# Kernel optimization log

Hardware: AMD Instinct MI355X
Metric: run time of the kernel (lower is better)

Reference implementation:

```python
import jax, jax.numpy as jnp
import numpy as np

B, S, D = 4, 2048, 1024
H = 16
DK = D // H  # 64, dim_k == dim_v
FF = 4096
EPS = 1e-5


def layer_norm(x, g, b):
    mu = jnp.mean(x, axis=-1, keepdims=True)
    var = jnp.mean(jnp.square(x - mu), axis=-1, keepdims=True)
    return (x - mu) * jax.lax.rsqrt(var + EPS) * g + b


def setup_inputs() -> dict:
    key = jax.random.key(0)
    ks = jax.random.split(key, 16)
    s = 0.02
    return {
        "src": jax.random.normal(ks[0], (B, S, D), jnp.float32),
        # per-head Q/K/V projections (stacked over heads)
        "wq": jax.random.normal(ks[1], (H, D, DK), jnp.float32) * s,
        "bq": jnp.zeros((H, DK), jnp.float32),
        "wk": jax.random.normal(ks[2], (H, D, DK), jnp.float32) * s,
        "bk": jnp.zeros((H, DK), jnp.float32),
        "wv": jax.random.normal(ks[3], (H, D, DK), jnp.float32) * s,
        "bv": jnp.zeros((H, DK), jnp.float32),
        # output projection: concat(H*DK) -> D
        "wo": jax.random.normal(ks[4], (H * DK, D), jnp.float32) * s,
        "bo": jnp.zeros((D,), jnp.float32),
        "ln1_g": jnp.ones((D,), jnp.float32),
        "ln1_b": jnp.zeros((D,), jnp.float32),
        # FFN
        "w1": jax.random.normal(ks[5], (D, FF), jnp.float32) * s,
        "b1": jnp.zeros((FF,), jnp.float32),
        "w2": jax.random.normal(ks[6], (FF, D), jnp.float32) * s,
        "b2": jnp.zeros((D,), jnp.float32),
        "ln2_g": jnp.ones((D,), jnp.float32),
        "ln2_b": jnp.zeros((D,), jnp.float32),
    }


def reference(src, wq, bq, wk, bk, wv, bv, wo, bo, ln1_g, ln1_b,
              w1, b1, w2, b2, ln2_g, ln2_b):
    # per-head projections: [B,S,D] x [H,D,K] -> [B,H,S,K]
    q = jnp.einsum('bsd,hdk->bhsk', src, wq) + bq[None, :, None, :]
    k = jnp.einsum('bsd,hdk->bhsk', src, wk) + bk[None, :, None, :]
    v = jnp.einsum('bsd,hdk->bhsk', src, wv) + bv[None, :, None, :]
    scale = 1.0 / jnp.sqrt(jnp.float32(DK))
    scores = jnp.einsum('bhsk,bhtk->bhst', q, k) * scale  # [B,H,S,S]
    attn = jax.nn.softmax(scores, axis=-1)
    o = jnp.einsum('bhst,bhtv->bhsv', attn, v)            # [B,H,S,DK]
    o = o.transpose(0, 2, 1, 3).reshape(B, S, H * DK)      # concat heads
    attn_out = o @ wo + bo
    x = layer_norm(src + attn_out, ln1_g, ln1_b)
    ff = jax.nn.relu(x @ w1 + b1) @ w2 + b2
    return layer_norm(x + ff, ln2_g, ln2_b)
```

## Files before the change

kernel.cpp:

```cpp
#include <hip/hip_runtime.h>

typedef __bf16 bf16;
typedef __bf16 bf16x8 __attribute__((ext_vector_type(8)));
typedef __bf16 bf16x4 __attribute__((ext_vector_type(4)));
typedef float  f32x4  __attribute__((ext_vector_type(4)));
typedef float  f32x16 __attribute__((ext_vector_type(16)));
typedef unsigned int u32;
typedef int i32x2 __attribute__((ext_vector_type(2)));
typedef int i32x4 __attribute__((ext_vector_type(4)));

#define NB 4
#define NS 2048
#define ND 1024
#define NH 16
#define NDK 64
#define NFF 4096
#define NM (NB*NS)

#define QSCALE 0.18033688f

__device__ __forceinline__ void load_lds16(const void* g, void* l) {
  __builtin_amdgcn_global_load_lds(
      (const __attribute__((address_space(1))) void*)g,
      (__attribute__((address_space(3))) void*)l, 16, 0, 0);
}

__device__ __forceinline__ u32 pack2(float a, float b) {
  union { bf16 h[2]; u32 u; } z;
  z.h[0] = (bf16)a; z.h[1] = (bf16)b;
  return z.u;
}

__device__ __forceinline__ i32x2 pswap(u32 a, u32 b) {
#if __has_builtin(__builtin_amdgcn_permlane32_swap)
  return __builtin_amdgcn_permlane32_swap((int)a, (int)b, false, false);
#else
  u32 x = a, y = b;
  asm volatile("v_permlane32_swap_b32 %0, %1" : "+v"(x), "+v"(y));
  i32x2 r; r[0] = (int)x; r[1] = (int)y; return r;
#endif
}

__global__ __launch_bounds__(256)
void cvt_f32_bf16(const float* __restrict__ in, bf16* __restrict__ out, int n) {
  int i = (blockIdx.x * 256 + threadIdx.x) * 4;
  if (i < n) {
    float4 v = *(const float4*)&in[i];
    bf16x4 o;
    o[0] = (bf16)v.x; o[1] = (bf16)v.y; o[2] = (bf16)v.z; o[3] = (bf16)v.w;
    *(bf16x4*)&out[i] = o;
  }
}

__global__ __launch_bounds__(256)
void transpose_cvt(const float* __restrict__ in, bf16* __restrict__ out,
                   int R, int C, size_t in_bs, size_t out_bs) {
  __shared__ float t[32][33];
  int bx = blockIdx.x, by = blockIdx.y, bz = blockIdx.z;
  const float* ip = in + (size_t)bz * in_bs + (size_t)(bx * 32) * C + by * 32;
  bf16* op = out + (size_t)bz * out_bs + (size_t)(by * 32) * R + bx * 32;
  int x = threadIdx.x & 31, y = threadIdx.x >> 5;
#pragma unroll
  for (int yy = 0; yy < 32; yy += 8)
    t[y + yy][x] = ip[(size_t)(y + yy) * C + x];
  __syncthreads();
#pragma unroll
  for (int yy = 0; yy < 32; yy += 8)
    op[(size_t)(y + yy) * R + x] = (bf16)t[x][y + yy];
}

__global__ __launch_bounds__(256)
void transpose_v(const bf16* __restrict__ v, bf16* __restrict__ vT) {
  __shared__ bf16 t[64][72];
  int st = blockIdx.x;
  int bh = blockIdx.y;
  const bf16* ip = v + ((size_t)bh * NS + st * 64) * NDK;
  bf16* op = vT + (size_t)bh * NDK * NS + st * 64;
  int tid = threadIdx.x;
#pragma unroll
  for (int c = tid; c < 512; c += 256) {
    int r = c >> 3, q = c & 7;
    bf16x8 d = *(const bf16x8*)&ip[(size_t)r * NDK + q * 8];
#pragma unroll
    for (int j = 0; j < 8; j++) t[r][q * 8 + j] = d[j];
  }
  __syncthreads();
#pragma unroll
  for (int c = tid; c < 512; c += 256) {
    int dv = c >> 3, sq = c & 7;
    bf16x8 d;
#pragma unroll
    for (int j = 0; j < 8; j++) d[j] = t[sq * 8 + j][dv];
    *(bf16x8*)&op[(size_t)dv * NS + sq * 8] = d;
  }
}

#define BAR()  __builtin_amdgcn_s_barrier()
#define LGKM0() do { asm volatile("s_waitcnt lgkmcnt(0)" ::: "memory"); \
                     __builtin_amdgcn_sched_barrier(0); } while (0)

template<int BN, int EPI>
__global__ __launch_bounds__(512, 2)
void gemm8p(const bf16* __restrict__ A, const bf16* __restrict__ Bt,
            const float* __restrict__ bias0, const float* __restrict__ bias1,
            const float* __restrict__ bias2, void* __restrict__ out0,
            int M, int N, int K) {
  constexpr int NFR = BN / 64;
  __shared__ __align__(16) bf16 lA[2][256 * 64];
  __shared__ __align__(16) bf16 lB[2][BN * 64];

  const int tid = threadIdx.x, lane = tid & 63, w = tid >> 6;
  const int wr = w >> 2, wn = w & 3;
  const int blane = lane & 15, glane = lane >> 4;

  const int nwg = gridDim.x;
  const int cpx = nwg >> 3;
  const int bid = blockIdx.x;
  const int swzb = (bid & 7) * cpx + (bid >> 3);
  const int gridM = M >> 8;
  const int bm = (swzb % gridM) * 256;
  const int bn = (swzb / gridM) * BN;

  f32x4 acc[8][NFR] = {};
  bf16x8 aF[8], bF[2 * NFR];

  auto stageA = [&](int kt, int h, int b) {
#pragma unroll
    for (int j = 0; j < 2; j++) {
      int ch = w * 128 + j * 64 + lane;
      int r = h * 128 + (ch >> 3), s = ch & 7;
      load_lds16(A + (size_t)(bm + r) * K + kt * 64 + ((s ^ (r & 7)) * 8),
                 &lA[b][(h * 1024 + ch) * 8]);
    }
  };
  auto stageB = [&](int kt, int h, int b) {
    if constexpr (BN == 256) {
#pragma unroll
      for (int j = 0; j < 2; j++) {
        int ch = w * 128 + j * 64 + lane;
        int r = h * 128 + (ch >> 3), s = ch & 7;
        load_lds16(Bt + (size_t)(bn + r) * K + kt * 64 + ((s ^ (r & 7)) * 8),
                   &lB[b][(h * 1024 + ch) * 8]);
      }
    } else {
      int ch = w * 64 + lane;
      int r = h * 64 + (ch >> 3), s = ch & 7;
      load_lds16(Bt + (size_t)(bn + r) * K + kt * 64 + ((s ^ (r & 7)) * 8),
                 &lB[b][(h * 512 + ch) * 8]);
    }
  };
  auto vmwait = [&]() {
    if constexpr (BN == 256) asm volatile("s_waitcnt vmcnt(6)" ::: "memory");
    else                     asm volatile("s_waitcnt vmcnt(4)" ::: "memory");
  };
  auto ldA = [&](int mh, int b) {
#pragma unroll
    for (int mf = 0; mf < 4; mf++)
#pragma unroll
      for (int ks = 0; ks < 2; ks++) {
        int r = wr * 128 + mh * 64 + mf * 16 + blane;
        int s = (ks * 4 + glane) ^ (r & 7);
        aF[mf * 2 + ks] = *(const bf16x8*)&lA[b][r * 64 + s * 8];
      }
  };
  auto ldBh = [&](int nh, int b) {
#pragma unroll
    for (int nq = 0; nq < NFR / 2; nq++)
#pragma unroll
      for (int ks = 0; ks < 2; ks++) {
        int nf = nh * (NFR / 2) + nq;
        int r = wn * (NFR * 16) + nf * 16 + blane;
        int s = (ks * 4 + glane) ^ (r & 7);
        bF[nf * 2 + ks] = *(const bf16x8*)&lB[b][r * 64 + s * 8];
      }
  };

#define MMAQ(mh, nh)  do {                                                  \
    __builtin_amdgcn_s_setprio(1);                                          \
    _Pragma("unroll")                                                       \
    for (int mf = 0; mf < 4; mf++)                                          \
      _Pragma("unroll")                                                     \
      for (int nq = 0; nq < NFR / 2; nq++)                                  \
        _Pragma("unroll")                                                   \
        for (int ks = 0; ks < 2; ks++)                                      \
          acc[(mh) * 4 + mf][(nh) * (NFR / 2) + nq] =                       \
            __builtin_amdgcn_mfma_f32_16x16x32_bf16(                        \
              aF[mf * 2 + ks], bF[((nh) * (NFR / 2) + nq) * 2 + ks],        \
              acc[(mh) * 4 + mf][(nh) * (NFR / 2) + nq], 0, 0, 0);          \
    __builtin_amdgcn_s_setprio(0);                                          \
  } while (0)

  stageB(0, 0, 0); stageB(0, 1, 0); stageA(0, 0, 0); stageA(0, 1, 0);
  stageB(1, 0, 1); stageB(1, 1, 1); stageA(1, 0, 1);
  vmwait();
  BAR();

  const int NT = K >> 6;
  for (int u = 0; u < NT; u += 2) {
    const int t2 = (u + 2 < NT) ? u + 2 : u;
    const int t3 = (u + 3 < NT) ? u + 3 : u + 1;
    ldA(0, 0); ldBh(0, 0);
    stageA(u + 1, 1, 1);
    BAR(); LGKM0(); MMAQ(0, 0); BAR();
    ldBh(1, 0);
    stageB(t2, 0, 0);
    BAR(); LGKM0(); MMAQ(0, 1); BAR();
    ldA(1, 0);
    stageB(t2, 1, 0);
    BAR(); LGKM0(); MMAQ(1, 1); BAR();
    stageA(t2, 0, 0);
    BAR(); MMAQ(1, 0); vmwait(); BAR();
    ldA(0, 1); ldBh(0, 1);
    stageA(t2, 1, 0);
    BAR(); LGKM0(); MMAQ(0, 0); BAR();
    ldBh(1, 1);
    stageB(t3, 0, 1);
    BAR(); LGKM0(); MMAQ(0, 1); BAR();
    ldA(1, 1);
    stageB(t3, 1, 1);
    BAR(); LGKM0(); MMAQ(1, 1); BAR();
    stageA(t3, 0, 1);
    BAR(); MMAQ(1, 0); vmwait(); BAR();
  }

#pragma unroll
  for (int am = 0; am < 8; am++) {
#pragma unroll
    for (int nf = 0; nf < NFR; nf++) {
      int col = bn + wn * (NFR * 16) + nf * 16 + blane;
      int rowb = bm + wr * 128 + (am >> 2) * 64 + (am & 3) * 16 + glane * 4;
      if (EPI == 0) {
        int sel = col >> 10;
        int hh = (col & 1023) >> 6;
        int dv = col & 63;
        const float* bp = (sel == 0) ? bias0 : (sel == 1) ? bias1 : bias2;
        float bias = bp[col & 1023];
        float sc = (sel == 0) ? QSCALE : 1.0f;
        bf16* outb = (bf16*)out0 + (size_t)sel * NB * NH * NS * NDK;
#pragma unroll
        for (int i = 0; i < 4; i++) {
          int row = rowb + i;
          int b_ = row >> 11, s_ = row & 2047;
          outb[(((size_t)(b_ * NH + hh) * NS + s_) * NDK) + dv] = (bf16)((acc[am][nf][i] + bias) * sc);
        }
      } else if (EPI == 1) {
        float bias = bias0[col];
#pragma unroll
        for (int i = 0; i < 4; i++) {
          float v = acc[am][nf][i] + bias;
          v = v > 0.f ? v : 0.f;
          ((bf16*)out0)[(size_t)(rowb + i) * N + col] = (bf16)v;
        }
      } else {
        float bias = bias0[col];
#pragma unroll
        for (int i = 0; i < 4; i++)
          ((float*)out0)[(size_t)(rowb + i) * N + col] = acc[am][nf][i] + bias;
      }
    }
  }
#undef MMAQ
}

__global__ __launch_bounds__(512)
void flash_attn7(const bf16* __restrict__ q, const bf16* __restrict__ k,
                 const bf16* __restrict__ vT, bf16* __restrict__ o) {
  __shared__ __align__(16) bf16 lK[2][64 * 64];
  __shared__ __align__(16) bf16 lV[2][64 * 64];
  const int tid = threadIdx.x, lane = tid & 63, w = tid >> 6;
  const int ql = lane & 31, hi = lane >> 5;

  const int id = blockIdx.x;
  const int xcd = id & 7, sseq = id >> 3;
  const int bh = xcd * 8 + (sseq >> 3);
  const int qt = sseq & 7;

  const size_t hb = (size_t)bh * NS * NDK;
  const int qrow = qt * 256 + w * 32 + ql;

  bf16x8 qf[4];
#pragma unroll
  for (int ks = 0; ks < 4; ks++)
    qf[ks] = *(const bf16x8*)&q[hb + (size_t)qrow * NDK + ks * 16 + hi * 8];

  const int sr = tid >> 3, sc = ((tid & 7) ^ (sr & 7)) * 8;
  const bf16* ksrc = k  + hb + (size_t)sr * NDK + sc;
  const bf16* vsrc = vT + hb + (size_t)sr * NS  + sc;

  f32x16 o0 = {}, o1 = {};
  float ls0 = 0.f, ls1 = 0.f, ls2 = 0.f, ls3 = 0.f;
  const int swz = (ql & 7) << 4;

  {
    i32x4 rk = *(const i32x4*)ksrc;
    i32x4 rv = *(const i32x4*)vsrc;
    *(i32x4*)&lK[0][tid * 8] = rk;
    *(i32x4*)&lV[0][tid * 8] = rv;
  }
  asm volatile("s_waitcnt lgkmcnt(0)" ::: "memory");
  __builtin_amdgcn_sched_barrier(0);
  __builtin_amdgcn_s_barrier();

  const char* lKc = (const char*)&lK[0][0];
  const char* lVc = (const char*)&lV[0][0];

  for (int t = 0; t < NS / 64; t++) {
    const int cur = t & 1;
    const char* Kb = lKc + cur * 8192;
    const char* Vb = lVc + cur * 8192;

    i32x4 nk, nv;
    const bool pf = (t < NS / 64 - 1);
    if (pf) {
      nk = *(const i32x4*)(ksrc + (size_t)(t + 1) * 64 * NDK);
      nv = *(const i32x4*)(vsrc + (t + 1) * 64);
    }

    f32x16 st0 = {}, st1 = {};
    __builtin_amdgcn_s_setprio(1);
#pragma unroll
    for (int ks = 0; ks < 4; ks++) {
      int byt = (32 * ks + 16 * hi) ^ swz;
      bf16x8 kf0 = *(const bf16x8*)(Kb + ql * 128 + byt);
      bf16x8 kf1 = *(const bf16x8*)(Kb + (32 + ql) * 128 + byt);
      st0 = __builtin_amdgcn_mfma_f32_32x32x16_bf16(kf0, qf[ks], st0, 0, 0, 0);
      st1 = __builtin_amdgcn_mfma_f32_32x32x16_bf16(kf1, qf[ks], st1, 0, 0, 0);
    }
    __builtin_amdgcn_s_setprio(0);

#pragma unroll
    for (int r = 0; r < 16; r += 4) {
      float p00 = exp2f(st0[r]),     p01 = exp2f(st0[r + 1]);
      float p02 = exp2f(st0[r + 2]), p03 = exp2f(st0[r + 3]);
      float p10 = exp2f(st1[r]),     p11 = exp2f(st1[r + 1]);
      float p12 = exp2f(st1[r + 2]), p13 = exp2f(st1[r + 3]);
      st0[r] = p00; st0[r + 1] = p01; st0[r + 2] = p02; st0[r + 3] = p03;
      st1[r] = p10; st1[r + 1] = p11; st1[r + 2] = p12; st1[r + 3] = p13;
      ls0 += p00 + p10; ls1 += p01 + p11;
      ls2 += p02 + p12; ls3 += p03 + p13;
    }

#pragma unroll
    for (int tt = 0; tt < 2; tt++) {
      f32x16 stv = (tt == 0) ? st0 : st1;
      u32 wv[8];
#pragma unroll
      for (int i = 0; i < 8; i++) wv[i] = pack2(stv[2 * i], stv[2 * i + 1]);
#pragma unroll
      for (int kk = 0; kk < 2; kk++) {
        const int base = 4 * kk;
        i32x2 e0 = pswap(wv[base + 0], wv[base + 2]);
        i32x2 e1 = pswap(wv[base + 1], wv[base + 3]);
        union { u32 u[4]; bf16x8 v; } pf_;
        pf_.u[0] = (u32)e0[0];
        pf_.u[1] = (u32)e1[0];
        pf_.u[2] = (u32)e0[1];
        pf_.u[3] = (u32)e1[1];
        const int ks = 2 * tt + kk;
        int vbyt = (32 * ks + 16 * hi) ^ swz;
        bf16x8 vf0 = *(const bf16x8*)(Vb + ql * 128 + vbyt);
        bf16x8 vf1 = *(const bf16x8*)(Vb + (32 + ql) * 128 + vbyt);
        __builtin_amdgcn_s_setprio(1);
        o0 = __builtin_amdgcn_mfma_f32_32x32x16_bf16(vf0, pf_.v, o0, 0, 0, 0);
        o1 = __builtin_amdgcn_mfma_f32_32x32x16_bf16(vf1, pf_.v, o1, 0, 0, 0);
        __builtin_amdgcn_s_setprio(0);
      }
    }

    if (pf) {
      *(i32x4*)&lK[cur ^ 1][tid * 8] = nk;
      *(i32x4*)&lV[cur ^ 1][tid * 8] = nv;
    }
    asm volatile("s_waitcnt lgkmcnt(0)" ::: "memory");
    __builtin_amdgcn_sched_barrier(0);
    __builtin_amdgcn_s_barrier();
  }

  float ls = (ls0 + ls1) + (ls2 + ls3);
  float lR;
  {
    i32x2 sr2 = pswap((u32)__float_as_int(ls), (u32)__float_as_int(ls));
    float lsp = __int_as_float(hi ? sr2[0] : sr2[1]);
    float lo_ = hi ? lsp : ls, hi_ = hi ? ls : lsp;
    lR = lo_ + hi_;
  }
  float invl = 1.0f / lR;
  int b_ = bh >> 4, h_ = bh & 15;
  bf16* ob = o + ((size_t)(b_ * NS + qrow) * (NH * NDK)) + h_ * NDK;
#pragma unroll
  for (int rp = 0; rp < 8; rp++) {
    int dv = 8 * (rp >> 1) + 2 * (rp & 1) + 4 * hi;
    *(u32*)&ob[dv]      = pack2(o0[2 * rp] * invl, o0[2 * rp + 1] * invl);
    *(u32*)&ob[dv + 32] = pack2(o1[2 * rp] * invl, o1[2 * rp + 1] * invl);
  }
}

template<int WB>
__global__ __launch_bounds__(256)
void ln_res(const float* __restrict__ a, const float* __restrict__ b,
            const float* __restrict__ g, const float* __restrict__ be,
            float* __restrict__ y, bf16* __restrict__ yb) {
  int row = blockIdx.x;
  int tid = threadIdx.x;
  const float4* a4 = (const float4*)(a + (size_t)row * ND);
  const float4* b4 = (const float4*)(b + (size_t)row * ND);
  float4 av = a4[tid], bv = b4[tid];
  float x0 = av.x + bv.x, x1 = av.y + bv.y, x2 = av.z + bv.z, x3 = av.w + bv.w;
  float s = x0 + x1 + x2 + x3;
  float qq_ = x0 * x0 + x1 * x1 + x2 * x2 + x3 * x3;
#pragma unroll
  for (int d = 1; d < 64; d <<= 1) { s += __shfl_xor(s, d); qq_ += __shfl_xor(qq_, d); }
  __shared__ float ss[4], sq[4];
  int w = tid >> 6, lane = tid & 63;
  if (lane == 0) { ss[w] = s; sq[w] = qq_; }
  __syncthreads();
  s = ss[0] + ss[1] + ss[2] + ss[3];
  qq_ = sq[0] + sq[1] + sq[2] + sq[3];
  float mu = s * (1.0f / ND);
  float var = qq_ * (1.0f / ND) - mu * mu;
  float rs = 1.0f / sqrtf(var + 1e-5f);
  const float4* g4 = (const float4*)g;
  const float4* e4 = (const float4*)be;
  float4 gv = g4[tid], ev = e4[tid];
  float o0 = (x0 - mu) * rs * gv.x + ev.x;
  float o1 = (x1 - mu) * rs * gv.y + ev.y;
  float o2 = (x2 - mu) * rs * gv.z + ev.z;
  float o3 = (x3 - mu) * rs * gv.w + ev.w;
  float4 ov = {o0, o1, o2, o3};
  *(float4*)(y + (size_t)row * ND + tid * 4) = ov;
  if (WB) {
    bf16x4 wv;
    wv[0] = (bf16)o0; wv[1] = (bf16)o1; wv[2] = (bf16)o2; wv[3] = (bf16)o3;
    *(bf16x4*)&yb[(size_t)row * ND + tid * 4] = wv;
  }
}

extern "C" void kernel_launch(void* const* d_in, const int* in_sizes, int n_in,
                              void* d_out, int out_size, void* d_ws, size_t ws_size,
                              hipStream_t stream) {
  const float* src = (const float*)d_in[0];
  const float* wq  = (const float*)d_in[1];
  const float* bq  = (const float*)d_in[2];
  const float* wk  = (const float*)d_in[3];
  const float* bk  = (const float*)d_in[4];
  const float* wv  = (const float*)d_in[5];
  const float* bv  = (const float*)d_in[6];
  const float* wo  = (const float*)d_in[7];
  const float* bo  = (const float*)d_in[8];
  const float* g1  = (const float*)d_in[9];
  const float* be1 = (const float*)d_in[10];
  const float* w1  = (const float*)d_in[11];
  const float* b1  = (const float*)d_in[12];
  const float* w2  = (const float*)d_in[13];
  const float* b2  = (const float*)d_in[14];
  const float* g2  = (const float*)d_in[15];
  const float* be2 = (const float*)d_in[16];

  char* ws = (char*)d_ws;
  bf16*  srcb  = (bf16*)(ws + 0);
  bf16*  wqkvT = (bf16*)(ws + 16777216);
  bf16*  woT   = (bf16*)(ws + 23068672);
  bf16*  w1T   = (bf16*)(ws + 25165824);
  bf16*  w2T   = (bf16*)(ws + 33554432);
  bf16*  qkv   = (bf16*)(ws + 41943040);
  bf16*  vT    = (bf16*)(ws + 92274688);
  bf16*  attno = (bf16*)(ws + 109051904);
  float* tmpf  = (float*)(ws + 125829120);
  float* x     = (float*)(ws + 159383552);
  bf16*  xb    = (bf16*)(ws + 192937984);
  bf16*  hbuf  = qkv;

  const size_t QKVSZ = (size_t)NB * NH * NS * NDK;

  cvt_f32_bf16<<<8192, 256, 0, stream>>>(src, srcb, NM * ND);
  transpose_cvt<<<dim3(32, 2, 16), 256, 0, stream>>>(wq, wqkvT,               1024, 64, 65536, 65536);
  transpose_cvt<<<dim3(32, 2, 16), 256, 0, stream>>>(wk, wqkvT + 1024 * 1024, 1024, 64, 65536, 65536);
  transpose_cvt<<<dim3(32, 2, 16), 256, 0, stream>>>(wv, wqkvT + 2048 * 1024, 1024, 64, 65536, 65536);
  transpose_cvt<<<dim3(32, 32, 1), 256, 0, stream>>>(wo, woT, 1024, 1024, 0, 0);
  transpose_cvt<<<dim3(32, 128, 1), 256, 0, stream>>>(w1, w1T, 1024, 4096, 0, 0);
  transpose_cvt<<<dim3(128, 32, 1), 256, 0, stream>>>(w2, w2T, 4096, 1024, 0, 0);

  gemm8p<256, 0><<<384, 512, 0, stream>>>(srcb, wqkvT, bq, bk, bv, qkv, NM, 3072, 1024);
  transpose_v<<<dim3(32, 64), 256, 0, stream>>>(qkv + 2 * QKVSZ, vT);
  flash_attn7<<<512, 512, 0, stream>>>(qkv, qkv + QKVSZ, vT, attno);
  gemm8p<128, 2><<<256, 512, 0, stream>>>(attno, woT, bo, nullptr, nullptr, tmpf, NM, 1024, 1024);
  ln_res<1><<<8192, 256, 0, stream>>>(src, tmpf, g1, be1, x, xb);
  gemm8p<256, 1><<<512, 512, 0, stream>>>(xb, w1T, b1, nullptr, nullptr, hbuf, NM, 4096, 1024);
  gemm8p<128, 2><<<256, 512, 0, stream>>>(hbuf, w2T, b2, nullptr, nullptr, tmpf, NM, 1024, 4096);
  ln_res<0><<<8192, 256, 0, stream>>>(x, tmpf, g2, be2, (float*)d_out, nullptr);
}
```

Measured before the change: 457.5 us.

## Store projection GEMM outputs in bf16 and shrink attention blocks to 256 threads

```diff
diff --git a/kernel.cpp b/kernel.cpp
--- a/kernel.cpp
+++ b/kernel.cpp
@@ -251,19 +251,24 @@
           v = v > 0.f ? v : 0.f;
           ((bf16*)out0)[(size_t)(rowb + i) * N + col] = (bf16)v;
         }
+      } else if (EPI == 2) {
+        float bias = bias0[col];
+#pragma unroll
+        for (int i = 0; i < 4; i++)
+          ((float*)out0)[(size_t)(rowb + i) * N + col] = acc[am][nf][i] + bias;
       } else {
         float bias = bias0[col];
 #pragma unroll
         for (int i = 0; i < 4; i++)
-          ((float*)out0)[(size_t)(rowb + i) * N + col] = acc[am][nf][i] + bias;
+          ((bf16*)out0)[(size_t)(rowb + i) * N + col] = (bf16)(acc[am][nf][i] + bias);
       }
     }
   }
 #undef MMAQ
 }
 
-__global__ __launch_bounds__(512)
-void flash_attn7(const bf16* __restrict__ q, const bf16* __restrict__ k,
+__global__ __launch_bounds__(256)
+void flash_attn8(const bf16* __restrict__ q, const bf16* __restrict__ k,
                  const bf16* __restrict__ vT, bf16* __restrict__ o) {
   __shared__ __align__(16) bf16 lK[2][64 * 64];
   __shared__ __align__(16) bf16 lV[2][64 * 64];
@@ -272,30 +277,37 @@
 
   const int id = blockIdx.x;
   const int xcd = id & 7, sseq = id >> 3;
-  const int bh = xcd * 8 + (sseq >> 3);
-  const int qt = sseq & 7;
+  const int bh = xcd * 8 + (sseq >> 4);
+  const int qt = sseq & 15;
 
   const size_t hb = (size_t)bh * NS * NDK;
-  const int qrow = qt * 256 + w * 32 + ql;
+  const int qrow = qt * 128 + w * 32 + ql;
 
   bf16x8 qf[4];
 #pragma unroll
   for (int ks = 0; ks < 4; ks++)
     qf[ks] = *(const bf16x8*)&q[hb + (size_t)qrow * NDK + ks * 16 + hi * 8];
 
-  const int sr = tid >> 3, sc = ((tid & 7) ^ (sr & 7)) * 8;
-  const bf16* ksrc = k  + hb + (size_t)sr * NDK + sc;
-  const bf16* vsrc = vT + hb + (size_t)sr * NS  + sc;
+  const int r0 = tid >> 3, s0 = ((tid & 7) ^ (r0 & 7)) * 8;
+  const int r1 = r0 + 32, s1 = ((tid & 7) ^ (r1 & 7)) * 8;
+  const bf16* k0 = k + hb + (size_t)r0 * NDK + s0;
+  const bf16* k1 = k + hb + (size_t)r1 * NDK + s1;
+  const bf16* v0 = vT + hb + (size_t)r0 * NS + s0;
+  const bf16* v1 = vT + hb + (size_t)r1 * NS + s1;
 
   f32x16 o0 = {}, o1 = {};
   float ls0 = 0.f, ls1 = 0.f, ls2 = 0.f, ls3 = 0.f;
   const int swz = (ql & 7) << 4;
 
   {
-    i32x4 rk = *(const i32x4*)ksrc;
-    i32x4 rv = *(const i32x4*)vsrc;
-    *(i32x4*)&lK[0][tid * 8] = rk;
-    *(i32x4*)&lV[0][tid * 8] = rv;
+    i32x4 a0 = *(const i32x4*)k0;
+    i32x4 a1 = *(const i32x4*)k1;
+    i32x4 b0 = *(const i32x4*)v0;
+    i32x4 b1 = *(const i32x4*)v1;
+    *(i32x4*)&lK[0][tid * 8] = a0;
+    *(i32x4*)&lK[0][(tid + 256) * 8] = a1;
+    *(i32x4*)&lV[0][tid * 8] = b0;
+    *(i32x4*)&lV[0][(tid + 256) * 8] = b1;
   }
   asm volatile("s_waitcnt lgkmcnt(0)" ::: "memory");
   __builtin_amdgcn_sched_barrier(0);
@@ -309,11 +321,15 @@
     const char* Kb = lKc + cur * 8192;
     const char* Vb = lVc + cur * 8192;
 
-    i32x4 nk, nv;
+    i32x4 nk0, nk1, nv0, nv1;
     const bool pf = (t < NS / 64 - 1);
     if (pf) {
-      nk = *(const i32x4*)(ksrc + (size_t)(t + 1) * 64 * NDK);
-      nv = *(const i32x4*)(vsrc + (t + 1) * 64);
+      const size_t ko = (size_t)(t + 1) * 64 * NDK;
+      const int vo = (t + 1) * 64;
+      nk0 = *(const i32x4*)(k0 + ko);
+      nk1 = *(const i32x4*)(k1 + ko);
+      nv0 = *(const i32x4*)(v0 + vo);
+      nv1 = *(const i32x4*)(v1 + vo);
     }
 
     f32x16 st0 = {}, st1 = {};
@@ -368,8 +384,10 @@
     }
 
     if (pf) {
-      *(i32x4*)&lK[cur ^ 1][tid * 8] = nk;
-      *(i32x4*)&lV[cur ^ 1][tid * 8] = nv;
+      *(i32x4*)&lK[cur ^ 1][tid * 8] = nk0;
+      *(i32x4*)&lK[cur ^ 1][(tid + 256) * 8] = nk1;
+      *(i32x4*)&lV[cur ^ 1][tid * 8] = nv0;
+      *(i32x4*)&lV[cur ^ 1][(tid + 256) * 8] = nv1;
     }
     asm volatile("s_waitcnt lgkmcnt(0)" ::: "memory");
     __builtin_amdgcn_sched_barrier(0);
@@ -397,15 +415,16 @@
 
 template<int WB>
 __global__ __launch_bounds__(256)
-void ln_res(const float* __restrict__ a, const float* __restrict__ b,
+void ln_res(const float* __restrict__ a, const bf16* __restrict__ b,
             const float* __restrict__ g, const float* __restrict__ be,
             float* __restrict__ y, bf16* __restrict__ yb) {
   int row = blockIdx.x;
   int tid = threadIdx.x;
   const float4* a4 = (const float4*)(a + (size_t)row * ND);
-  const float4* b4 = (const float4*)(b + (size_t)row * ND);
-  float4 av = a4[tid], bv = b4[tid];
-  float x0 = av.x + bv.x, x1 = av.y + bv.y, x2 = av.z + bv.z, x3 = av.w + bv.w;
+  float4 av = a4[tid];
+  bf16x4 bv = *(const bf16x4*)(b + (size_t)row * ND + tid * 4);
+  float x0 = av.x + (float)bv[0], x1 = av.y + (float)bv[1];
+  float x2 = av.z + (float)bv[2], x3 = av.w + (float)bv[3];
   float s = x0 + x1 + x2 + x3;
   float qq_ = x0 * x0 + x1 * x1 + x2 * x2 + x3 * x3;
 #pragma unroll
@@ -465,7 +484,7 @@
   bf16*  qkv   = (bf16*)(ws + 41943040);
   bf16*  vT    = (bf16*)(ws + 92274688);
   bf16*  attno = (bf16*)(ws + 109051904);
-  float* tmpf  = (float*)(ws + 125829120);
+  bf16*  tmpb  = (bf16*)(ws + 125829120);
   float* x     = (float*)(ws + 159383552);
   bf16*  xb    = (bf16*)(ws + 192937984);
   bf16*  hbuf  = qkv;
@@ -482,10 +501,10 @@
 
   gemm8p<256, 0><<<384, 512, 0, stream>>>(srcb, wqkvT, bq, bk, bv, qkv, NM, 3072, 1024);
   transpose_v<<<dim3(32, 64), 256, 0, stream>>>(qkv + 2 * QKVSZ, vT);
-  flash_attn7<<<512, 512, 0, stream>>>(qkv, qkv + QKVSZ, vT, attno);
-  gemm8p<128, 2><<<256, 512, 0, stream>>>(attno, woT, bo, nullptr, nullptr, tmpf, NM, 1024, 1024);
-  ln_res<1><<<8192, 256, 0, stream>>>(src, tmpf, g1, be1, x, xb);
+  flash_attn8<<<1024, 256, 0, stream>>>(qkv, qkv + QKVSZ, vT, attno);
+  gemm8p<128, 3><<<256, 512, 0, stream>>>(attno, woT, bo, nullptr, nullptr, tmpb, NM, 1024, 1024);
+  ln_res<1><<<8192, 256, 0, stream>>>(src, tmpb, g1, be1, x, xb);
   gemm8p<256, 1><<<512, 512, 0, stream>>>(xb, w1T, b1, nullptr, nullptr, hbuf, NM, 4096, 1024);
-  gemm8p<128, 2><<<256, 512, 0, stream>>>(hbuf, w2T, b2, nullptr, nullptr, tmpf, NM, 1024, 4096);
-  ln_res<0><<<8192, 256, 0, stream>>>(x, tmpf, g2, be2, (float*)d_out, nullptr);
-}
+  gemm8p<128, 3><<<256, 512, 0, stream>>>(hbuf, w2T, b2, nullptr, nullptr, tmpb, NM, 1024, 4096);
+  ln_res<0><<<8192, 256, 0, stream>>>(x, tmpb, g2, be2, (float*)d_out, nullptr);
+}
```

Measured after the change: 472.7 us. 3.3% more time.
